# Optimization experiments

Hardware: AMD Instinct MI355X
Metric: run time of the kernel (lower is better)

The kernel has to match this reference:

```python
import jax, jax.numpy as jnp
import numpy as np

N_NODES = 100000
N_EDGES = 3200000
NUM_FEATURES = 128
NH = 64
NUM_CLASSES = 32
K = 6
K_MIX = 2
W_SCALE = 0.05


def setup_inputs() -> dict:
    key = jax.random.key(0)
    ks = jax.random.split(key, 16)
    inp = {
        "x": jax.random.normal(ks[0], (N_NODES, NUM_FEATURES), jnp.float32),
        "edge_index": jax.random.randint(ks[1], (2, N_EDGES), 0, N_NODES, jnp.int32),
        "W0": jax.random.normal(ks[2], (K, NUM_FEATURES, NH), jnp.float32) * W_SCALE,
        "b0": jnp.zeros((NH,), jnp.float32),
        "Ws0": jax.random.normal(ks[3], (1, NUM_FEATURES, NH), jnp.float32) * W_SCALE,
        "bs0": jnp.zeros((NH,), jnp.float32),
        "W1": jax.random.normal(ks[4], (K, NH, NH), jnp.float32) * W_SCALE,
        "b1": jnp.zeros((NH,), jnp.float32),
        "Ws1": jax.random.normal(ks[5], (1, NH, NH), jnp.float32) * W_SCALE,
        "bs1": jnp.zeros((NH,), jnp.float32),
        "W2": jax.random.normal(ks[6], (K, NH, NH), jnp.float32) * W_SCALE,
        "b2": jnp.zeros((NH,), jnp.float32),
        "Ws2": jax.random.normal(ks[7], (1, NH, NH), jnp.float32) * W_SCALE,
        "bs2": jnp.zeros((NH,), jnp.float32),
        "Wmix": jax.random.normal(ks[8], (K_MIX, NH + NUM_FEATURES, NUM_CLASSES), jnp.float32) * W_SCALE,
        "bmix": jnp.zeros((NUM_CLASSES,), jnp.float32),
    }
    return inp


def _cheb_conv(h, src, dst, norm_w, Wk, b, n_nodes):
    # Chebyshev recursion with L_hat = -D^{-1/2} A D^{-1/2} (lambda_max = 2,
    # sym normalization -> self-loop terms of the scaled Laplacian cancel).
    def prop(t):  # L_hat @ t : one sparse hop (gather -> scale -> scatter-add)
        return -jax.ops.segment_sum(norm_w[:, None] * t[src], dst, num_segments=n_nodes)

    k_hops = Wk.shape[0]
    Tx0 = h
    out = Tx0 @ Wk[0]
    if k_hops > 1:
        Tx1 = prop(Tx0)
        out = out + Tx1 @ Wk[1]
        for k in range(2, k_hops):
            Tx2 = 2.0 * prop(Tx1) - Tx0
            out = out + Tx2 @ Wk[k]
            Tx0, Tx1 = Tx1, Tx2
    return out + b


def reference(x, edge_index, W0, b0, Ws0, bs0, W1, b1, Ws1, bs1,
              W2, b2, Ws2, bs2, Wmix, bmix):
    n = x.shape[0]
    src, dst = edge_index[0], edge_index[1]
    deg = jax.ops.segment_sum(jnp.ones_like(src, jnp.float32), dst, num_segments=n)
    dis = jnp.where(deg > 0, jax.lax.rsqrt(jnp.maximum(deg, 1.0)), 0.0)
    norm_w = dis[src] * dis[dst]  # per-edge sym-normalized weight

    h = x
    for (W, b, Ws, bs) in ((W0, b0, Ws0, bs0), (W1, b1, Ws1, bs1), (W2, b2, Ws2, bs2)):
        # Kipfblock (relu, dropout is identity in eval mode) + K=1 skip ChebConv
        h = jax.nn.relu(_cheb_conv(h, src, dst, norm_w, W, b, n)) \
            + _cheb_conv(h, src, dst, norm_w, Ws, bs, n)
    h = jnp.concatenate((h, x), axis=1)  # in/out skip connection
    return _cheb_conv(h, src, dst, norm_w, Wmix, bmix, n)
```

## Files before the change

### kernel.cpp

```cpp
#include <hip/hip_runtime.h>
#include <hip/hip_bf16.h>
#include <cstdio>
#include <cstdint>

typedef __hip_bfloat16 bf16;
typedef __attribute__((ext_vector_type(8)))  short short8v;
typedef __attribute__((ext_vector_type(4)))  float f32x4;

static __device__ __forceinline__ float b2f(bf16 v){ return __bfloat162float(v); }
static __device__ __forceinline__ bf16  f2b(float v){ return __float2bfloat16(v); }
static __device__ __forceinline__ float ldf(const float* p){ return *p; }
static __device__ __forceinline__ float ldf(const bf16* p){ return b2f(*p); }

static __device__ __forceinline__ float bl(uint32_t u){ union{uint32_t i; float f;} c; c.i = u<<16;          return c.f; }
static __device__ __forceinline__ float bh(uint32_t u){ union{uint32_t i; float f;} c; c.i = u & 0xffff0000u; return c.f; }
static __device__ __forceinline__ uint32_t pk(float lo, float hi){
  bf16 a=f2b(lo), b=f2b(hi);
  uint16_t ai=*reinterpret_cast<uint16_t*>(&a), bi=*reinterpret_cast<uint16_t*>(&b);
  return ((uint32_t)bi<<16) | ai;
}
static __device__ __forceinline__ void ld2(const bf16* p, unsigned i32, float& lo, float& hi){
  uint32_t u = reinterpret_cast<const uint32_t*>(p)[i32]; lo=bl(u); hi=bh(u);
}
static __device__ __forceinline__ void ld2(const float* p, unsigned i32, float& lo, float& hi){
  float2 v = reinterpret_cast<const float2*>(p)[i32]; lo=v.x; hi=v.y;
}
static __device__ __forceinline__ void st2(bf16* p, unsigned i32, float lo, float hi){
  reinterpret_cast<uint32_t*>(p)[i32] = pk(lo,hi);
}
static __device__ __forceinline__ void st2(float* p, unsigned i32, float lo, float hi){
  reinterpret_cast<float2*>(p)[i32] = make_float2(lo,hi);
}


__global__ void k_count(const int* __restrict__ dst, int* __restrict__ deg, int E){
  int e = blockIdx.x*256 + threadIdx.x;
  if(e<E) atomicAdd(&deg[dst[e]], 1);
}

__global__ void k_scan1(const int* __restrict__ deg, int* __restrict__ rp1, int* __restrict__ bsums, int N){
  __shared__ int s[256];
  int i = blockIdx.x*256 + threadIdx.x;
  int v = (i<N)? deg[i] : 0;
  s[threadIdx.x]=v; __syncthreads();
  for(int off=1; off<256; off<<=1){
    int t = (threadIdx.x>=off)? s[threadIdx.x-off] : 0;
    __syncthreads();
    s[threadIdx.x]+=t;
    __syncthreads();
  }
  if(i<N) rp1[i]=s[threadIdx.x];
  if(threadIdx.x==255) bsums[blockIdx.x]=s[255];
}

__global__ void k_scan2(const int* __restrict__ bsums, int* __restrict__ boffs, int NB){
  __shared__ int s[512];
  int x=threadIdx.x;
  int v = (x<NB)? bsums[x] : 0;
  s[x]=v; __syncthreads();
  for(int off=1; off<512; off<<=1){
    int t=(x>=off)? s[x-off]:0; __syncthreads();
    s[x]+=t; __syncthreads();
  }
  if(x<NB) boffs[x]=s[x]-v;
}

__global__ void k_scan3(int* __restrict__ row_ptr, const int* __restrict__ boffs,
                        const int* __restrict__ deg, float* __restrict__ dis, float* __restrict__ dinv, int N){
  int i = blockIdx.x*256+threadIdx.x;
  if(i<N){
    row_ptr[i+1] += boffs[blockIdx.x];
    int d = deg[i];
    dis[i]  = (d>0)? rsqrtf((float)d) : 0.f;
    dinv[i] = (d>0)? sqrtf((float)d)  : 0.f;
    if(i==0) row_ptr[0]=0;
  }
}

__global__ void k_fill(const int* __restrict__ src, const int* __restrict__ dst,
                       const int* __restrict__ row_ptr, int* __restrict__ deg,
                       int* __restrict__ csr_src, int E){
  int e = blockIdx.x*256+threadIdx.x;
  if(e<E){
    int d = dst[e];
    int pos = row_ptr[d] + atomicAdd(&deg[d],-1) - 1;
    csr_src[pos] = src[e];
  }
}


__global__ void k_hist(const int* __restrict__ dst, int* __restrict__ chunk_hist,
                       int* __restrict__ btot, int E, int nbuk, int epc){
  __shared__ int h[1600];
  for(int i=threadIdx.x;i<nbuk;i+=256) h[i]=0;
  __syncthreads();
  int base=blockIdx.x*epc, end=min(base+epc,E);
  for(int e=base+(int)threadIdx.x; e<end; e+=256) atomicAdd(&h[dst[e]>>6],1);
  __syncthreads();
  for(int i=threadIdx.x;i<nbuk;i+=256){
    int hv=h[i];
    chunk_hist[(size_t)i*256 + blockIdx.x]=hv;
    if(hv) atomicAdd(&btot[i],hv);
  }
}

__global__ void k_bfix(const int* __restrict__ binc, const int* __restrict__ btot,
                       const int* __restrict__ boffs, int* __restrict__ bbase, int nbuk){
  int i=blockIdx.x*256+threadIdx.x;
  if(i<nbuk) bbase[i] = binc[i] + boffs[i>>8] - btot[i];
}

__global__ void k_cscan(int* __restrict__ chunk_hist, const int* __restrict__ bbase, int nbuk){
  __shared__ int s[256];
  int b=blockIdx.x; if(b>=nbuk) return;
  int x=threadIdx.x;
  int v=chunk_hist[(size_t)b*256+x];
  s[x]=v; __syncthreads();
  for(int off=1; off<256; off<<=1){
    int t=(x>=off)? s[x-off]:0; __syncthreads();
    s[x]+=t; __syncthreads();
  }
  chunk_hist[(size_t)b*256+x] = s[x]-v + bbase[b];
}

__global__ void k_bscat(const int* __restrict__ src, const int* __restrict__ dst,
                        const int* __restrict__ cbase, uint2* __restrict__ ebuf,
                        int E, int nbuk, int epc){
  __shared__ int cur[1600];
  for(int i=threadIdx.x;i<nbuk;i+=256) cur[i]=cbase[(size_t)i*256 + blockIdx.x];
  __syncthreads();
  int base=blockIdx.x*epc, end=min(base+epc,E);
  for(int e=base+(int)threadIdx.x; e<end; e+=256){
    int d=dst[e], s=src[e];
    int p=atomicAdd(&cur[d>>6],1);
    ebuf[p]=make_uint2((unsigned)s,(unsigned)d);
  }
}

__global__ void k_fill2(const uint2* __restrict__ ebuf, const int* __restrict__ row_ptr,
                        int* __restrict__ deg, int* __restrict__ csr_src, int E){
  int e = blockIdx.x*256+threadIdx.x;
  if(e<E){
    uint2 p = ebuf[e];
    int d=(int)p.y;
    int pos = row_ptr[d] + atomicAdd(&deg[d],-1) - 1;
    csr_src[pos] = (int)p.x;
  }
}

__global__ void k_prep(const float* __restrict__ W0, const float* __restrict__ Ws0,
                       const float* __restrict__ W1, const float* __restrict__ Ws1,
                       const float* __restrict__ W2, const float* __restrict__ Ws2,
                       const float* __restrict__ Wmix,
                       bf16* __restrict__ WT0, bf16* __restrict__ WT1,
                       bf16* __restrict__ WT2, bf16* __restrict__ WTm){
  int idx = blockIdx.x*256 + threadIdx.x;
  if(idx < 57344){
    int w = idx >> 13, r = idx & 8191;
    int k = r >> 6, n = r & 63;
    float v = (w==0)? Ws0[(k<<6)+n] : W0[(((6-w)<<7) + k)*64 + n];
    WT0[(size_t)((w<<6)+n)*136 + k] = f2b(v);
  } else if(idx < 57344+28672){
    int i2 = idx - 57344;
    int w = i2 >> 12, r = i2 & 4095;
    int k = r >> 6, n = r & 63;
    float v = (w==0)? Ws1[(k<<6)+n] : W1[(((6-w)<<6) + k)*64 + n];
    WT1[(size_t)((w<<6)+n)*72 + k] = f2b(v);
  } else if(idx < 57344+2*28672){
    int i2 = idx - (57344+28672);
    int w = i2 >> 12, r = i2 & 4095;
    int k = r >> 6, n = r & 63;
    float v = (w==0)? Ws2[(k<<6)+n] : W2[(((6-w)<<6) + k)*64 + n];
    WT2[(size_t)((w<<6)+n)*72 + k] = f2b(v);
  } else if(idx < 57344+2*28672+12288){
    int i2 = idx - (57344+2*28672);
    int n = i2 / 192, k = i2 % 192;
    float v = (n<32)? Wmix[k*32 + n] : Wmix[6144 + k*32 + (n-32)];
    WTm[(size_t)n*200 + k] = f2b(v);
  }
}

template<int K, int NW, int AMODE>
__global__ __launch_bounds__(256,2) void k_mfma(
    const bf16* __restrict__ Ab, const float* __restrict__ Af, const bf16* __restrict__ WT,
    bf16* __restrict__ O0, bf16* __restrict__ O1, bf16* __restrict__ O2, bf16* __restrict__ O3,
    bf16* __restrict__ O4, bf16* __restrict__ O5, bf16* __restrict__ O6,
    float* __restrict__ Zf, const float* __restrict__ dis, int M)
{
  constexpr int Kp = K + 8;
  static_assert(Kp % 8 == 0, "Kp must keep 16B alignment");
  constexpr int NS = K / 32;
  constexpr int NSLOT = (NW>1) ? 2 : 1;
  __shared__ short sA[128][Kp];
  __shared__ short sW[NSLOT][64][Kp];

  const int t    = threadIdx.x;
  const int m0   = blockIdx.x * 128;
  const int l    = t & 63;
  const int wid  = t >> 6;
  const int wrow = (wid >> 1) * 64;
  const int wcol = (wid & 1) * 32;
  const int l4   = l & 15;
  const int lk8  = (l >> 4) * 8;

  bf16* const Ol[7] = {O0,O1,O2,O3,O4,O5,O6};
  const short8v szero = {0,0,0,0,0,0,0,0};
  const f32x4   fzero = {0.f,0.f,0.f,0.f};

  constexpr int WCH = (64*Kp)/8;
  constexpr int WIT = (WCH + 255)/256;
  short8v wreg[WIT];
  auto loadW = [&](int w){
    #pragma unroll
    for(int it=0; it<WIT; ++it){
      int c = t + it*256;
      if(c < WCH) wreg[it] = *reinterpret_cast<const short8v*>(&WT[(size_t)w*(64*Kp) + (size_t)c*8]);
    }
  };
  auto writeW = [&](int slot){
    short* base = &sW[slot][0][0];
    #pragma unroll
    for(int it=0; it<WIT; ++it){
      int c = t + it*256;
      if(c < WCH) *reinterpret_cast<short8v*>(base + (size_t)c*8) = wreg[it];
    }
  };

  loadW(0);

  {
    constexpr int CPR = K/8;
    #pragma unroll
    for(int it=0; it<(128*CPR)/256; ++it){
      int c = t + it*256;
      int row = c / CPR, j = c % CPR;
      int m = m0 + row;
      short8v v = szero;
      if(m < M){
        if constexpr(AMODE==0){
          v = *reinterpret_cast<const short8v*>(&Ab[(size_t)m*K + j*8]);
        } else if constexpr(AMODE==1){
          float4 f0 = *reinterpret_cast<const float4*>(&Af[(size_t)m*K + j*8]);
          float4 f1 = *reinterpret_cast<const float4*>(&Af[(size_t)m*K + j*8 + 4]);
          bf16* hp = reinterpret_cast<bf16*>(&v);
          hp[0]=f2b(f0.x); hp[1]=f2b(f0.y); hp[2]=f2b(f0.z); hp[3]=f2b(f0.w);
          hp[4]=f2b(f1.x); hp[5]=f2b(f1.y); hp[6]=f2b(f1.z); hp[7]=f2b(f1.w);
        } else {
          if(j < 8){
            v = *reinterpret_cast<const short8v*>(&Ab[(size_t)m*64 + j*8]);
          } else {
            float4 f0 = *reinterpret_cast<const float4*>(&Af[(size_t)m*128 + (j-8)*8]);
            float4 f1 = *reinterpret_cast<const float4*>(&Af[(size_t)m*128 + (j-8)*8 + 4]);
            bf16* hp = reinterpret_cast<bf16*>(&v);
            hp[0]=f2b(f0.x); hp[1]=f2b(f0.y); hp[2]=f2b(f0.z); hp[3]=f2b(f0.w);
            hp[4]=f2b(f1.x); hp[5]=f2b(f1.y); hp[6]=f2b(f1.z); hp[7]=f2b(f1.w);
          }
        }
      }
      *reinterpret_cast<short8v*>(&sA[row][j*8]) = v;
    }
  }

  writeW(0);
  __syncthreads();

  short8v af[4][(NS>0)?NS:1];
  if constexpr(NW > 1){
    #pragma unroll
    for(int rt=0; rt<4; ++rt)
      #pragma unroll
      for(int s=0; s<NS; ++s)
        af[rt][s] = *reinterpret_cast<const short8v*>(&sA[wrow + rt*16 + l4][s*32 + lk8]);
  }

  #pragma unroll
  for(int w=0; w<NW; ++w){
    if(w+1 < NW) loadW(w+1);

    f32x4 acc[4][2];
    #pragma unroll
    for(int rt=0; rt<4; ++rt){ acc[rt][0]=fzero; acc[rt][1]=fzero; }

    const short* wb = &sW[(NW>1)?(w&1):0][0][0];
    #pragma unroll
    for(int s=0; s<NS; ++s){
      short8v b0 = *reinterpret_cast<const short8v*>(wb + (size_t)(wcol +      l4)*Kp + s*32 + lk8);
      short8v b1 = *reinterpret_cast<const short8v*>(wb + (size_t)(wcol + 16 + l4)*Kp + s*32 + lk8);
      #pragma unroll
      for(int rt=0; rt<4; ++rt){
        short8v a = (NW>1) ? af[rt][s]
                  : *reinterpret_cast<const short8v*>(&sA[wrow + rt*16 + l4][s*32 + lk8]);
        acc[rt][0] = __builtin_amdgcn_mfma_f32_16x16x32_bf16(a, b0, acc[rt][0], 0,0,0);
        acc[rt][1] = __builtin_amdgcn_mfma_f32_16x16x32_bf16(a, b1, acc[rt][1], 0,0,0);
      }
    }

    if(w+1 < NW){ writeW((w+1)&1); __syncthreads(); }

    #pragma unroll
    for(int rt=0; rt<4; ++rt){
      #pragma unroll
      for(int r=0; r<4; ++r){
        int row = m0 + wrow + rt*16 + ((l>>4)<<2) + r;
        if(row < M){
          if constexpr(AMODE != 2){
            float sc = 1.f;
            if(NW>1 && w==1) sc = dis[row];
            #pragma unroll
            for(int ct=0; ct<2; ++ct){
              float vv = acc[rt][ct][r] * sc;
              Ol[w][(size_t)row*64 + wcol + ct*16 + l4] = f2b(vv);
            }
          } else {
            float dm = dis[row];
            #pragma unroll
            for(int ct=0; ct<2; ++ct){
              int col = wcol + ct*16 + l4;
              float vv = acc[rt][ct][r];
              if(col < 32) Zf[(size_t)row*32 + col] = vv;
              else         O0[(size_t)row*32 + (col-32)] = f2b(vv*dm);
            }
          }
        }
      }
    }
  }
}

template<int F, int MODE, typename ZT, typename OT>
__global__ __launch_bounds__(256) void k_prop(const int* __restrict__ row_ptr, const int* __restrict__ csr_src,
    const float* __restrict__ dis, const float* __restrict__ dinv, const bf16* __restrict__ BinS,
    const ZT* __restrict__ Z, const bf16* __restrict__ BsubS,
    const float* __restrict__ bias, const bf16* __restrict__ Zs, const float* __restrict__ bias2,
    OT* __restrict__ out, int N){
  constexpr int L   = F/2;
  constexpr int NPB = 256/L;
  int v = blockIdx.x*NPB + threadIdx.x/L;
  if(v>=N) return;
  int f2 = threadIdx.x % L;
  const uint32_t* __restrict__ B32 = reinterpret_cast<const uint32_t*>(BinS);
  int e0=row_ptr[v], e1=row_ptr[v+1];
  unsigned idx32 = (unsigned)v*L + f2;

  float zL, zH; ld2(Z, idx32, zL, zH);
  float bsL=0.f, bsH=0.f;
  if constexpr(MODE==1 || MODE==2){
    uint32_t bu = reinterpret_cast<const uint32_t*>(BsubS)[idx32]; bsL=bl(bu); bsH=bh(bu);
  }
  float biL=0.f, biH=0.f;
  if constexpr(MODE>=2){
    float2 bv = reinterpret_cast<const float2*>(bias)[f2]; biL=bv.x; biH=bv.y;
  }
  float zsL=0.f, zsH=0.f, b2L=0.f, b2H=0.f;
  if constexpr(MODE==2){
    uint32_t su = reinterpret_cast<const uint32_t*>(Zs)[idx32]; zsL=bl(su); zsH=bh(su);
    float2 b2v = reinterpret_cast<const float2*>(bias2)[f2]; b2L=b2v.x; b2H=b2v.y;
  }
  float dv = dis[v];
  float di = dinv[v];

  float aL=0.f, aH=0.f;
  int e=e0;
  for(; e+L<=e1; e+=L){
    int si = csr_src[e + f2];
    #pragma unroll
    for(int c=0; c<L/16; ++c){
      int s[16];
      #pragma unroll
      for(int j=0;j<16;++j) s[j] = __shfl(si, c*16+j, L);
      uint32_t u[16];
      #pragma unroll
      for(int j=0;j<16;++j) u[j]=B32[(unsigned)s[j]*L + f2];
      #pragma unroll
      for(int j=0;j<16;++j){ aL+=bl(u[j]); aH+=bh(u[j]); }
    }
  }
  if(e+16<=e1){
    int s[16];
    #pragma unroll
    for(int j=0;j<16;++j) s[j]=csr_src[e+j];
    uint32_t u[16];
    #pragma unroll
    for(int j=0;j<16;++j) u[j]=B32[(unsigned)s[j]*L + f2];
    #pragma unroll
    for(int j=0;j<16;++j){ aL+=bl(u[j]); aH+=bh(u[j]); }
    e+=16;
  }
  if(e+8<=e1){
    int s[8];
    #pragma unroll
    for(int j=0;j<8;++j) s[j]=csr_src[e+j];
    uint32_t u[8];
    #pragma unroll
    for(int j=0;j<8;++j) u[j]=B32[(unsigned)s[j]*L + f2];
    #pragma unroll
    for(int j=0;j<8;++j){ aL+=bl(u[j]); aH+=bh(u[j]); }
    e+=8;
  }
  if(e<e1){
    #pragma unroll
    for(int j=0;j<8;++j){
      int idx=e+j;
      int s=csr_src[idx<e1 ? idx : e0];
      uint32_t uu=B32[(unsigned)s*L + f2];
      if(idx<e1){ aL+=bl(uu); aH+=bh(uu); }
    }
  }
  aL*=dv; aH*=dv;
  float rL, rH;
  if constexpr(MODE==0){ rL = zL - 2.f*aL;              rH = zH - 2.f*aH; }
  else if constexpr(MODE==1){ rL = zL - 2.f*aL - bsL*di; rH = zH - 2.f*aH - bsH*di; }
  else if constexpr(MODE==2){
    float tL = zL - aL - bsL*di + biL;
    float tH = zH - aH - bsH*di + biH;
    rL = fmaxf(tL,0.f) + zsL + b2L;
    rH = fmaxf(tH,0.f) + zsH + b2H;
  } else { rL = zL - aL + biL; rH = zH - aH + biH; }
  if constexpr(MODE<=1) st2(out, idx32, dv*rL, dv*rH);
  else                  st2(out, idx32, rL, rH);
}


extern "C" void kernel_launch(void* const* d_in, const int* in_sizes, int n_in,
                              void* d_out, int out_size, void* d_ws, size_t ws_size,
                              hipStream_t stream) {
  const int N = in_sizes[0]/128;
  const int E = in_sizes[1]/2;

  const float* x    = (const float*)d_in[0];
  const int*   ei   = (const int*  )d_in[1];
  const float* W0   = (const float*)d_in[2];
  const float* b0   = (const float*)d_in[3];
  const float* Ws0  = (const float*)d_in[4];
  const float* bs0  = (const float*)d_in[5];
  const float* W1   = (const float*)d_in[6];
  const float* b1   = (const float*)d_in[7];
  const float* Ws1  = (const float*)d_in[8];
  const float* bs1  = (const float*)d_in[9];
  const float* W2   = (const float*)d_in[10];
  const float* b2   = (const float*)d_in[11];
  const float* Ws2  = (const float*)d_in[12];
  const float* bs2  = (const float*)d_in[13];
  const float* Wmix = (const float*)d_in[14];
  const float* bmix = (const float*)d_in[15];
  float* out = (float*)d_out;

  const int* src = ei;
  const int* dst = ei + E;

  size_t off=0;
  char* ws=(char*)d_ws;
  auto alloc=[&](size_t bytes)->void*{ void* p = ws+off; off=(off+bytes+255)&~(size_t)255; return p; };
  int*   csr_src = (int*)  alloc((size_t)E*4);
  int*   row_ptr = (int*)  alloc((size_t)(N+1)*4);
  int*   deg     = (int*)  alloc((size_t)N*4);
  float* dis     = (float*)alloc((size_t)N*4);
  float* dinv    = (float*)alloc((size_t)N*4);
  int*   bsums   = (int*)  alloc(2048);
  int*   boffs   = (int*)  alloc(2048);
  bf16*  Z0      = (bf16*) alloc((size_t)N*64*2);
  bf16*  Z1      = (bf16*) alloc((size_t)N*64*2);
  bf16*  Z2      = (bf16*) alloc((size_t)N*64*2);
  bf16*  Z3      = (bf16*) alloc((size_t)N*64*2);
  bf16*  Z4      = (bf16*) alloc((size_t)N*64*2);
  bf16*  Zsb     = (bf16*) alloc((size_t)N*64*2);
  bf16*  P0s     = (bf16*) alloc((size_t)N*64*2);
  bf16*  P1s     = (bf16*) alloc((size_t)N*64*2);
  bf16*  P2s     = (bf16*) alloc((size_t)N*64*2);
  bf16*  hA      = (bf16*) alloc((size_t)N*64*2);
  bf16*  hB      = (bf16*) alloc((size_t)N*64*2);
  bf16*  WT0     = (bf16*) alloc((size_t)7*64*136*2);
  bf16*  WT1     = (bf16*) alloc((size_t)7*64*72*2);
  bf16*  WT2     = (bf16*) alloc((size_t)7*64*72*2);
  bf16*  WTm     = (bf16*) alloc((size_t)64*200*2);
  if(off > ws_size){
    fprintf(stderr, "kernel_launch: workspace too small: need %zu, have %zu\n", off, ws_size);
    return;
  }

  const int NB   = (N+255)/256;
  const int gE   = (E+255)/256;
  const int gM   = (N+127)/128;
  const int gP64 = (N+7)/8;
  const int gP32 = (N+15)/16;

  const int nbuk = (N+63)>>6;
  const int NB2  = (nbuk+255)/256;
  const int epc  = (E+255)/256;
  const bool fast_fill = (nbuk <= 1600);
  char*  gs         = (char*)Z0;
  uint2* ebuf       = (uint2*)gs;
  int*   chunk_hist = (int*)(gs + (((size_t)E*8 + 255) & ~(size_t)255));
  int*   binc       = chunk_hist + (size_t)nbuk*256;
  int*   btot       = binc + nbuk;
  int*   bbase      = btot + nbuk;

  k_prep<<<496,256,0,stream>>>(W0,Ws0,W1,Ws1,W2,Ws2,Wmix, WT0,WT1,WT2,WTm);

  hipMemsetAsync(deg, 0, (size_t)N*4, stream);
  k_count<<<gE,256,0,stream>>>(dst, deg, E);
  if(fast_fill){
    hipMemsetAsync(btot, 0, (size_t)nbuk*4, stream);
    k_hist<<<256,256,0,stream>>>(dst, chunk_hist, btot, E, nbuk, epc);
    k_scan1<<<NB2,256,0,stream>>>(btot, binc, bsums, nbuk);
    k_scan2<<<1,512,0,stream>>>(bsums, boffs, NB2);
    k_bfix<<<NB2,256,0,stream>>>(binc, btot, boffs, bbase, nbuk);
    k_cscan<<<nbuk,256,0,stream>>>(chunk_hist, bbase, nbuk);
  }
  k_scan1<<<NB,256,0,stream>>>(deg, row_ptr+1, bsums, N);
  k_scan2<<<1,512,0,stream>>>(bsums, boffs, NB);
  k_scan3<<<NB,256,0,stream>>>(row_ptr, boffs, deg, dis, dinv, N);
  if(fast_fill){
    k_bscat<<<256,256,0,stream>>>(src, dst, chunk_hist, ebuf, E, nbuk, epc);
    k_fill2<<<gE,256,0,stream>>>(ebuf, row_ptr, deg, csr_src, E);
  } else {
    k_fill<<<gE,256,0,stream>>>(src, dst, row_ptr, deg, csr_src, E);
  }

  auto PROPS=[&](const float* b, const float* bs_, bf16* hout){
    k_prop<64,0,bf16,bf16><<<gP64,256,0,stream>>>(row_ptr,csr_src,dis,dinv,P0s,Z4,nullptr,nullptr,nullptr,nullptr,P1s,N);
    k_prop<64,1,bf16,bf16><<<gP64,256,0,stream>>>(row_ptr,csr_src,dis,dinv,P1s,Z3,P0s,nullptr,nullptr,nullptr,P2s,N);
    k_prop<64,1,bf16,bf16><<<gP64,256,0,stream>>>(row_ptr,csr_src,dis,dinv,P2s,Z2,P1s,nullptr,nullptr,nullptr,P0s,N);
    k_prop<64,1,bf16,bf16><<<gP64,256,0,stream>>>(row_ptr,csr_src,dis,dinv,P0s,Z1,P2s,nullptr,nullptr,nullptr,P1s,N);
    k_prop<64,2,bf16,bf16><<<gP64,256,0,stream>>>(row_ptr,csr_src,dis,dinv,P1s,Z0,P0s,b,Zsb,bs_,hout,N);
  };

  k_mfma<128,7,1><<<gM,256,0,stream>>>(nullptr, x, WT0, Zsb,P0s,Z4,Z3,Z2,Z1,Z0, nullptr, dis, N);
  PROPS(b0, bs0, hA);
  k_mfma<64,7,0><<<gM,256,0,stream>>>(hA, nullptr, WT1, Zsb,P0s,Z4,Z3,Z2,Z1,Z0, nullptr, dis, N);
  PROPS(b1, bs1, hB);
  k_mfma<64,7,0><<<gM,256,0,stream>>>(hB, nullptr, WT2, Zsb,P0s,Z4,Z3,Z2,Z1,Z0, nullptr, dis, N);
  PROPS(b2, bs2, hA);

  float* Zmixf = (float*)Z1;
  k_mfma<192,1,2><<<gM,256,0,stream>>>(hA, x, WTm, P0s,nullptr,nullptr,nullptr,nullptr,nullptr,nullptr, Zmixf, dis, N);
  k_prop<32,3,float,float><<<gP32,256,0,stream>>>(row_ptr,csr_src,dis,dinv,P0s,Zmixf,nullptr,bmix,nullptr,nullptr,out,N);
}
```

Baseline: 1.596 ms.

## Build CSR per 64-node bucket using shared-memory atomics after bucket scatter

After edges are scattered into 64-node dst buckets, a per-bucket kernel counts degrees with LDS atomics, which replaces the global-atomic count pass over all edges. A second per-bucket kernel fills csr_src using LDS cursors instead of global atomicAdd on deg. This removes two passes of global atomics over the edge list but reorders the CSR build stages. Bucket-size imbalance could leave some blocks with more work.

New measurement: 1.381 ms. -13.5%, faster.

```diff
diff --git a/kernel.cpp b/kernel.cpp
--- a/kernel.cpp
+++ b/kernel.cpp
@@ -36,6 +36,16 @@
 __global__ void k_count(const int* __restrict__ dst, int* __restrict__ deg, int E){
   int e = blockIdx.x*256 + threadIdx.x;
   if(e<E) atomicAdd(&deg[dst[e]], 1);
+}
+__global__ void k_fill(const int* __restrict__ src, const int* __restrict__ dst,
+                       const int* __restrict__ row_ptr, int* __restrict__ deg,
+                       int* __restrict__ csr_src, int E){
+  int e = blockIdx.x*256+threadIdx.x;
+  if(e<E){
+    int d = dst[e];
+    int pos = row_ptr[d] + atomicAdd(&deg[d],-1) - 1;
+    csr_src[pos] = src[e];
+  }
 }
 
 __global__ void k_scan1(const int* __restrict__ deg, int* __restrict__ rp1, int* __restrict__ bsums, int N){
@@ -77,18 +87,6 @@
   }
 }
 
-__global__ void k_fill(const int* __restrict__ src, const int* __restrict__ dst,
-                       const int* __restrict__ row_ptr, int* __restrict__ deg,
-                       int* __restrict__ csr_src, int E){
-  int e = blockIdx.x*256+threadIdx.x;
-  if(e<E){
-    int d = dst[e];
-    int pos = row_ptr[d] + atomicAdd(&deg[d],-1) - 1;
-    csr_src[pos] = src[e];
-  }
-}
-
-
 __global__ void k_hist(const int* __restrict__ dst, int* __restrict__ chunk_hist,
                        int* __restrict__ btot, int E, int nbuk, int epc){
   __shared__ int h[1600];
@@ -137,14 +135,37 @@
   }
 }
 
-__global__ void k_fill2(const uint2* __restrict__ ebuf, const int* __restrict__ row_ptr,
-                        int* __restrict__ deg, int* __restrict__ csr_src, int E){
-  int e = blockIdx.x*256+threadIdx.x;
-  if(e<E){
-    uint2 p = ebuf[e];
-    int d=(int)p.y;
-    int pos = row_ptr[d] + atomicAdd(&deg[d],-1) - 1;
-    csr_src[pos] = (int)p.x;
+__global__ void k_degf(const uint2* __restrict__ ebuf, const int* __restrict__ bbase,
+                       const int* __restrict__ btot, int* __restrict__ deg, int N){
+  __shared__ int cnt[64];
+  int b=blockIdx.x;
+  if(threadIdx.x<64) cnt[threadIdx.x]=0;
+  __syncthreads();
+  int e0=bbase[b], e1=e0+btot[b];
+  for(int e=e0+(int)threadIdx.x; e<e1; e+=256) atomicAdd(&cnt[ebuf[e].y & 63],1);
+  __syncthreads();
+  int n=b*64+(int)threadIdx.x;
+  if(threadIdx.x<64 && n<N) deg[n]=cnt[threadIdx.x];
+}
+
+__global__ void k_fill3(const uint2* __restrict__ ebuf, const int* __restrict__ bbase,
+                        const int* __restrict__ btot, const int* __restrict__ row_ptr,
+                        int* __restrict__ csr_src, int N){
+  __shared__ int cur[64];
+  __shared__ int rp[64];
+  int b=blockIdx.x;
+  int n=b*64+(int)threadIdx.x;
+  if(threadIdx.x<64){
+    cur[threadIdx.x]=0;
+    rp[threadIdx.x] = (n<N)? row_ptr[n] : 0;
+  }
+  __syncthreads();
+  int e0=bbase[b], e1=e0+btot[b];
+  for(int e=e0+(int)threadIdx.x; e<e1; e+=256){
+    uint2 p=ebuf[e];
+    int li=(int)(p.y & 63);
+    int idx=atomicAdd(&cur[li],1);
+    csr_src[rp[li]+idx]=(int)p.x;
   }
 }
 
@@ -497,8 +518,6 @@
 
   k_prep<<<496,256,0,stream>>>(W0,Ws0,W1,Ws1,W2,Ws2,Wmix, WT0,WT1,WT2,WTm);
 
-  hipMemsetAsync(deg, 0, (size_t)N*4, stream);
-  k_count<<<gE,256,0,stream>>>(dst, deg, E);
   if(fast_fill){
     hipMemsetAsync(btot, 0, (size_t)nbuk*4, stream);
     k_hist<<<256,256,0,stream>>>(dst, chunk_hist, btot, E, nbuk, epc);
@@ -506,14 +525,18 @@
     k_scan2<<<1,512,0,stream>>>(bsums, boffs, NB2);
     k_bfix<<<NB2,256,0,stream>>>(binc, btot, boffs, bbase, nbuk);
     k_cscan<<<nbuk,256,0,stream>>>(chunk_hist, bbase, nbuk);
-  }
-  k_scan1<<<NB,256,0,stream>>>(deg, row_ptr+1, bsums, N);
-  k_scan2<<<1,512,0,stream>>>(bsums, boffs, NB);
-  k_scan3<<<NB,256,0,stream>>>(row_ptr, boffs, deg, dis, dinv, N);
-  if(fast_fill){
     k_bscat<<<256,256,0,stream>>>(src, dst, chunk_hist, ebuf, E, nbuk, epc);
-    k_fill2<<<gE,256,0,stream>>>(ebuf, row_ptr, deg, csr_src, E);
+    k_degf<<<nbuk,256,0,stream>>>(ebuf, bbase, btot, deg, N);
+    k_scan1<<<NB,256,0,stream>>>(deg, row_ptr+1, bsums, N);
+    k_scan2<<<1,512,0,stream>>>(bsums, boffs, NB);
+    k_scan3<<<NB,256,0,stream>>>(row_ptr, boffs, deg, dis, dinv, N);
+    k_fill3<<<nbuk,256,0,stream>>>(ebuf, bbase, btot, row_ptr, csr_src, N);
   } else {
+    hipMemsetAsync(deg, 0, (size_t)N*4, stream);
+    k_count<<<gE,256,0,stream>>>(dst, deg, E);
+    k_scan1<<<NB,256,0,stream>>>(deg, row_ptr+1, bsums, N);
+    k_scan2<<<1,512,0,stream>>>(bsums, boffs, NB);
+    k_scan3<<<NB,256,0,stream>>>(row_ptr, boffs, deg, dis, dinv, N);
     k_fill<<<gE,256,0,stream>>>(src, dst, row_ptr, deg, csr_src, E);
   }
 
```
